# Optimization experiments

Hardware: AMD Instinct MI355X
Metric: run time of the kernel (lower is better)

## Reference

```python
import jax, jax.numpy as jnp
import numpy as np


def _haar_coeffs(x, s):
    # 2x2 depthwise Haar conv at stride s, no padding.
    # Output spatial size = floor((H-2)/s)+1 = len(range(0, H-1, s)).
    H, W = x.shape[-2], x.shape[-1]
    x00 = x[..., 0:H - 1:s, 0:W - 1:s]
    x01 = x[..., 0:H - 1:s, 1:W:s]
    x10 = x[..., 1:H:s, 0:W - 1:s]
    x11 = x[..., 1:H:s, 1:W:s]
    ll = (x00 + x01 + x10 + x11) * 0.25
    lh = (x00 + x01 - x10 - x11) * 0.25
    hl = (x00 - x01 + x10 - x11) * 0.25
    hh = (x00 - x01 - x10 + x11) * 0.25
    return ll, lh, hl, hh


def _resize_hw(x, H, W):
    # bilinear, half-pixel centers == torch align_corners=False (upsampling)
    return jax.image.resize(x, x.shape[:-2] + (H, W), method='linear')


def setup_inputs() -> dict:
    key = jax.random.key(0)
    x = jax.random.normal(key, (8, 64, 256, 256), dtype=jnp.float32)
    return {"x": x, "level": 2}


def reference(x, level):
    B, C, H, W = x.shape
    low_freq = x
    high_freq = jnp.zeros_like(x)
    for l in range(level):
        stride = 2 ** l
        if H // stride < 2 or W // stride < 2:
            break
        ll, lh, hl, hh = _haar_coeffs(low_freq, stride)
        current_high = jnp.abs(lh) + jnp.abs(hl) + jnp.abs(hh)
        high_freq = high_freq + _resize_hw(current_high, H, W)
        low_freq = _resize_hw(ll, H, W)
    if level > 0:
        high_freq = high_freq / level
    return (low_freq, high_freq)
```

## Files before the change

kernel.cpp:

```cpp
#include <hip/hip_runtime.h>


constexpr int IW = 256, IH = 256;

__device__ __forceinline__ float lerpf(float a, float b, float t) {
  return a + t * (b - a);
}

__global__ __launch_bounds__(256)
void haar_fused(const float* __restrict__ x,
                float* __restrict__ out_low,
                float* __restrict__ out_high) {
  const int bc = blockIdx.y;
  const int ti = blockIdx.x >> 2;
  const int tj = blockIdx.x & 3;
  const int i0 = ti * 64, j0 = tj * 64;
  const int tid = threadIdx.x;
  const int lane = tid & 63;
  const int wid = tid >> 6;
  const float c512 = 1.0f / 512.0f;

  __shared__ float sX[70 * 72];
  __shared__ float sLL1[69 * 69];
  __shared__ float sCH1[65 * 65];
  __shared__ float sLL2[34 * 34];
  __shared__ float sCH2[34 * 34];

  const float* xc = x + (size_t)bc * (IH * IW);

  const int colbase = min(max(j0 - 4, 0), IW - 72);
  const int soff = colbase - j0 + 4;
  for (int idx = tid; idx < 70 * 18; idx += 256) {
    int r = idx / 18;
    int c4 = idx - r * 18;
    int gslot = 4 * c4 + soff;
    if (gslot >= 0 && gslot <= 68) {
      int gr = min(max(i0 - 3 + r, 0), IH - 1);
      const float4 v = *reinterpret_cast<const float4*>(&xc[gr * IW + colbase + 4 * c4]);
      *reinterpret_cast<float4*>(&sX[r * 72 + gslot]) = v;
    }
  }
  if (soff != 0) {
    __syncthreads();
    if (tid < 70) {
      if (soff > 0) {
        float v = sX[tid * 72 + 4];
        sX[tid * 72 + 0] = v; sX[tid * 72 + 1] = v;
        sX[tid * 72 + 2] = v; sX[tid * 72 + 3] = v;
      } else {
        float v = sX[tid * 72 + 67];
        sX[tid * 72 + 68] = v; sX[tid * 72 + 69] = v;
        sX[tid * 72 + 70] = v; sX[tid * 72 + 71] = v;
      }
    }
  }
  __syncthreads();

  {
    int r0 = wid * 18;
    int r1 = min(r0 + 18, 69);
    int xc0 = lane + 1;
    float a = sX[r0 * 72 + xc0], b = sX[r0 * 72 + xc0 + 1];
    float s = a + b, d = a - b;
    for (int xr = r0; xr < r1; ++xr) {
      float a2 = sX[(xr + 1) * 72 + xc0], b2 = sX[(xr + 1) * 72 + xc0 + 1];
      float s2 = a2 + b2, d2 = a2 - b2;
      sLL1[xr * 69 + lane] = 0.25f * (s + s2);
      float lh = 0.25f * (s - s2);
      float hl = 0.25f * (d + d2);
      float hh = 0.25f * (d - d2);
      float ch = fabsf(lh) + fabsf(hl) + fabsf(hh);
      if (lane >= 2 && (unsigned)(xr - 2) <= 64u)
        sCH1[(xr - 2) * 65 + (lane - 2)] = ch;
      s = s2; d = d2;
    }
  }
  for (int f = tid; f < 5 * 69; f += 256) {
    int q = f / 69;
    int xr = f - q * 69;
    int xc0 = 65 + q;
    float a = sX[xr * 72 + xc0], b = sX[xr * 72 + xc0 + 1];
    float a2 = sX[(xr + 1) * 72 + xc0], b2 = sX[(xr + 1) * 72 + xc0 + 1];
    float s = a + b, d = a - b, s2 = a2 + b2, d2 = a2 - b2;
    sLL1[xr * 69 + (xc0 - 1)] = 0.25f * (s + s2);
    if (xc0 <= 67 && (unsigned)(xr - 2) <= 64u) {
      float lh = 0.25f * (s - s2);
      float hl = 0.25f * (d + d2);
      float hh = 0.25f * (d - d2);
      sCH1[(xr - 2) * 65 + (xc0 - 3)] = fabsf(lh) + fabsf(hl) + fabsf(hh);
    }
  }
  __syncthreads();

  {
    int fcc = lane;
    int C = j0 - 2 + fcc;
    float ccf = (float)C - (float)(2 * C + 1) * c512;
    float fc = fminf(fmaxf(ccf, 0.0f), 254.0f) - (float)(C - 1);
    int r0 = wid * 17, r1 = r0 + 17;
    float A = sLL1[r0 * 69 + fcc], B = sLL1[r0 * 69 + fcc + 1];
    float hz = A + fc * (B - A);
    for (int fr = r0; fr < r1; ++fr) {
      float A2 = sLL1[(fr + 1) * 69 + fcc], B2 = sLL1[(fr + 1) * 69 + fcc + 1];
      float hz2 = A2 + fc * (B2 - A2);
      int R = i0 - 2 + fr;
      float crf = (float)R - (float)(2 * R + 1) * c512;
      float fw = fminf(fmaxf(crf, 0.0f), 254.0f) - (float)(R - 1);
      sX[fr * 68 + fcc] = hz + fw * (hz2 - hz);
      hz = hz2;
    }
  }
  for (int f = tid; f < 4 * 68; f += 256) {
    int q = f / 68;
    int fr = f - q * 68;
    int fcc = 64 + q;
    int C = j0 - 2 + fcc;
    float ccf = (float)C - (float)(2 * C + 1) * c512;
    float fc = fminf(fmaxf(ccf, 0.0f), 254.0f) - (float)(C - 1);
    float A = sLL1[fr * 69 + fcc], B = sLL1[fr * 69 + fcc + 1];
    float A2 = sLL1[(fr + 1) * 69 + fcc], B2 = sLL1[(fr + 1) * 69 + fcc + 1];
    int R = i0 - 2 + fr;
    float crf = (float)R - (float)(2 * R + 1) * c512;
    float fw = fminf(fmaxf(crf, 0.0f), 254.0f) - (float)(R - 1);
    float hz = A + fc * (B - A);
    float hz2 = A2 + fc * (B2 - A2);
    sX[fr * 68 + fcc] = hz + fw * (hz2 - hz);
  }
  __syncthreads();

  for (int idx = tid; idx < 34 * 32; idx += 256) {
    int pr = idx >> 5, pc = idx & 31;
    int base = (2 * pr) * 68 + 2 * pc;
    float f00 = sX[base], f01 = sX[base + 1];
    float f10 = sX[base + 68], f11 = sX[base + 69];
    float sa = f00 + f01, sb = f10 + f11;
    float da = f00 - f01, db = f10 - f11;
    sLL2[pr * 34 + pc] = 0.25f * (sa + sb);
    sCH2[pr * 34 + pc] =
        fabsf(0.25f * (sa - sb)) + fabsf(0.25f * (da + db)) + fabsf(0.25f * (da - db));
  }
  if (tid < 68) {
    int pr = tid >> 1, pc = 32 + (tid & 1);
    int base = (2 * pr) * 68 + 2 * pc;
    float f00 = sX[base], f01 = sX[base + 1];
    float f10 = sX[base + 68], f11 = sX[base + 69];
    float sa = f00 + f01, sb = f10 + f11;
    float da = f00 - f01, db = f10 - f11;
    sLL2[pr * 34 + pc] = 0.25f * (sa + sb);
    sCH2[pr * 34 + pc] =
        fabsf(0.25f * (sa - sb)) + fabsf(0.25f * (da + db)) + fabsf(0.25f * (da - db));
  }
  __syncthreads();

  {
    const int cg = tid & 15, rb = tid >> 4;
    const int cbase = 4 * cg;
    const int q0 = (j0 >> 1) - 1;
    const int p0 = (i0 >> 1) - 1;
    float fc1[4], fc2[4];
#pragma unroll
    for (int m = 0; m < 4; ++m) {
      int jj = j0 + cbase + m;
      float ccf = (float)jj - (float)(2 * jj + 1) * c512;
      fc1[m] = fminf(fmaxf(ccf, 0.0f), 254.0f) - (float)(jj - 1);
      int qu = (jj - 1) >> 1;
      fc2[m] = fminf(fmaxf(0.5f * (float)jj - 0.25f, 0.0f), 127.0f) - (float)qu;
    }
    const int qs0 = ((j0 + cbase - 1) >> 1) - q0;
    const size_t obase = (size_t)bc * (IH * IW);

#pragma unroll
    for (int k = 0; k < 4; ++k) {
      int r = rb + 16 * k;
      int i = i0 + r;
      float crf = (float)i - (float)(2 * i + 1) * c512;
      float fr1 = fminf(fmaxf(crf, 0.0f), 254.0f) - (float)(i - 1);
      int pu = (i - 1) >> 1;
      float fr2 = fminf(fmaxf(0.5f * (float)i - 0.25f, 0.0f), 127.0f) - (float)pu;
      int ps = pu - p0;

      const float* chA = &sCH1[r * 65 + cbase];
      const float* chB = chA + 65;
      const float* llA = &sLL2[ps * 34 + qs0];
      const float* llB = llA + 34;
      const float* c2A = &sCH2[ps * 34 + qs0];
      const float* c2B = c2A + 34;

      float av[5], bv[5];
#pragma unroll
      for (int m = 0; m < 5; ++m) { av[m] = chA[m]; bv[m] = chB[m]; }
      float lav[4], lbv[4], gav[4], gbv[4];
#pragma unroll
      for (int m = 0; m < 4; ++m) {
        lav[m] = llA[m]; lbv[m] = llB[m];
        gav[m] = c2A[m]; gbv[m] = c2B[m];
      }

      float lo[4], hi[4];
#pragma unroll
      for (int m = 0; m < 4; ++m) {
        const int k2 = (m == 0) ? 0 : (m == 3 ? 2 : 1);
        float h1 = lerpf(lerpf(av[m], av[m + 1], fc1[m]),
                         lerpf(bv[m], bv[m + 1], fc1[m]), fr1);
        float l_ = lerpf(lerpf(lav[k2], lav[k2 + 1], fc2[m]),
                         lerpf(lbv[k2], lbv[k2 + 1], fc2[m]), fr2);
        float h2 = lerpf(lerpf(gav[k2], gav[k2 + 1], fc2[m]),
                         lerpf(gbv[k2], gbv[k2 + 1], fc2[m]), fr2);
        lo[m] = l_;
        hi[m] = 0.5f * (h1 + h2);
      }
      float4 lowv = make_float4(lo[0], lo[1], lo[2], lo[3]);
      float4 highv = make_float4(hi[0], hi[1], hi[2], hi[3]);
      size_t off = obase + (size_t)i * IW + (j0 + cbase);
      *reinterpret_cast<float4*>(&out_low[off]) = lowv;
      *reinterpret_cast<float4*>(&out_high[off]) = highv;
    }
  }
}

extern "C" void kernel_launch(void* const* d_in, const int* in_sizes, int n_in,
                              void* d_out, int out_size, void* d_ws, size_t ws_size,
                              hipStream_t stream) {
  (void)in_sizes; (void)n_in; (void)d_ws; (void)ws_size; (void)out_size;
  const float* x = (const float*)d_in[0];
  float* out_low = (float*)d_out;
  float* out_high = out_low + (size_t)8 * 64 * 256 * 256;

  dim3 grid(16, 512, 1);
  dim3 block(256, 1, 1);
  haar_fused<<<grid, block, 0, stream>>>(x, out_low, out_high);
}
```

Before: 442.2 us.

## Shrink row tile to 32 and fuse level-1 LL with bilinear resize

```diff
diff --git a/kernel.cpp b/kernel.cpp
--- a/kernel.cpp
+++ b/kernel.cpp
@@ -14,27 +14,27 @@
   const int bc = blockIdx.y;
   const int ti = blockIdx.x >> 2;
   const int tj = blockIdx.x & 3;
-  const int i0 = ti * 64, j0 = tj * 64;
+  const int i0 = ti * 32, j0 = tj * 64;
   const int tid = threadIdx.x;
   const int lane = tid & 63;
   const int wid = tid >> 6;
   const float c512 = 1.0f / 512.0f;
 
-  __shared__ float sX[70 * 72];
-  __shared__ float sLL1[69 * 69];
-  __shared__ float sCH1[65 * 65];
-  __shared__ float sLL2[34 * 34];
-  __shared__ float sCH2[34 * 34];
+  __shared__ float sX[38 * 72];
+  __shared__ float sCH1[33 * 68];
+  __shared__ float sLF1[36 * 68];
+  __shared__ float sLL2[18 * 34];
+  __shared__ float sCH2[18 * 34];
 
   const float* xc = x + (size_t)bc * (IH * IW);
 
   const int colbase = min(max(j0 - 4, 0), IW - 72);
   const int soff = colbase - j0 + 4;
-  for (int idx = tid; idx < 70 * 18; idx += 256) {
+  for (int idx = tid; idx < 38 * 18; idx += 256) {
     int r = idx / 18;
     int c4 = idx - r * 18;
     int gslot = 4 * c4 + soff;
-    if (gslot >= 0 && gslot <= 68) {
+    if ((unsigned)gslot <= 68u) {
       int gr = min(max(i0 - 3 + r, 0), IH - 1);
       const float4 v = *reinterpret_cast<const float4*>(&xc[gr * IW + colbase + 4 * c4]);
       *reinterpret_cast<float4*>(&sX[r * 72 + gslot]) = v;
@@ -42,7 +42,7 @@
   }
   if (soff != 0) {
     __syncthreads();
-    if (tid < 70) {
+    if (tid < 38) {
       if (soff > 0) {
         float v = sX[tid * 72 + 4];
         sX[tid * 72 + 0] = v; sX[tid * 72 + 1] = v;
@@ -57,106 +57,94 @@
   __syncthreads();
 
   {
-    int r0 = wid * 18;
-    int r1 = min(r0 + 18, 69);
-    int xc0 = lane + 1;
-    float a = sX[r0 * 72 + xc0], b = sX[r0 * 72 + xc0 + 1];
+    const int r0 = (wid < 3) ? wid * 9 : 27;
+    const int r1 = (wid < 3) ? r0 + 9 : 33;
+    const int xs = lane + 3;
+    float a = sX[(r0 + 2) * 72 + xs], b = sX[(r0 + 2) * 72 + xs + 1];
     float s = a + b, d = a - b;
-    for (int xr = r0; xr < r1; ++xr) {
-      float a2 = sX[(xr + 1) * 72 + xc0], b2 = sX[(xr + 1) * 72 + xc0 + 1];
+    for (int r = r0; r < r1; ++r) {
+      float a2 = sX[(r + 3) * 72 + xs], b2 = sX[(r + 3) * 72 + xs + 1];
       float s2 = a2 + b2, d2 = a2 - b2;
-      sLL1[xr * 69 + lane] = 0.25f * (s + s2);
-      float lh = 0.25f * (s - s2);
-      float hl = 0.25f * (d + d2);
-      float hh = 0.25f * (d - d2);
-      float ch = fabsf(lh) + fabsf(hl) + fabsf(hh);
-      if (lane >= 2 && (unsigned)(xr - 2) <= 64u)
-        sCH1[(xr - 2) * 65 + (lane - 2)] = ch;
+      sCH1[r * 68 + lane] =
+          0.25f * (fabsf(s - s2) + fabsf(d + d2) + fabsf(d - d2));
       s = s2; d = d2;
     }
   }
-  for (int f = tid; f < 5 * 69; f += 256) {
-    int q = f / 69;
-    int xr = f - q * 69;
-    int xc0 = 65 + q;
-    float a = sX[xr * 72 + xc0], b = sX[xr * 72 + xc0 + 1];
-    float a2 = sX[(xr + 1) * 72 + xc0], b2 = sX[(xr + 1) * 72 + xc0 + 1];
+  if (tid < 33) {
+    int r = tid;
+    float a = sX[(r + 2) * 72 + 67], b = sX[(r + 2) * 72 + 68];
+    float a2 = sX[(r + 3) * 72 + 67], b2 = sX[(r + 3) * 72 + 68];
     float s = a + b, d = a - b, s2 = a2 + b2, d2 = a2 - b2;
-    sLL1[xr * 69 + (xc0 - 1)] = 0.25f * (s + s2);
-    if (xc0 <= 67 && (unsigned)(xr - 2) <= 64u) {
-      float lh = 0.25f * (s - s2);
-      float hl = 0.25f * (d + d2);
-      float hh = 0.25f * (d - d2);
-      sCH1[(xr - 2) * 65 + (xc0 - 3)] = fabsf(lh) + fabsf(hl) + fabsf(hh);
-    }
-  }
-  __syncthreads();
+    sCH1[r * 68 + 64] =
+        0.25f * (fabsf(s - s2) + fabsf(d + d2) + fabsf(d - d2));
+  }
 
   {
-    int fcc = lane;
-    int C = j0 - 2 + fcc;
+    const int l = lane;
+    const int C = j0 - 2 + l;
     float ccf = (float)C - (float)(2 * C + 1) * c512;
-    float fc = fminf(fmaxf(ccf, 0.0f), 254.0f) - (float)(C - 1);
-    int r0 = wid * 17, r1 = r0 + 17;
-    float A = sLL1[r0 * 69 + fcc], B = sLL1[r0 * 69 + fcc + 1];
-    float hz = A + fc * (B - A);
-    for (int fr = r0; fr < r1; ++fr) {
-      float A2 = sLL1[(fr + 1) * 69 + fcc], B2 = sLL1[(fr + 1) * 69 + fcc + 1];
-      float hz2 = A2 + fc * (B2 - A2);
+    const float t = fminf(fmaxf(ccf, 0.0f), 254.0f) - (float)(C - 1);
+    const int r0 = wid * 9;
+    const float* rowp = &sX[r0 * 72 + l + 1];
+    float xa = rowp[0], xm = rowp[1], xb = rowp[2];
+    float h0 = 0.5f * ((1.0f - t) * xa + xm + t * xb);
+    xa = rowp[72]; xm = rowp[73]; xb = rowp[74];
+    float h1 = 0.5f * ((1.0f - t) * xa + xm + t * xb);
+    for (int fr = r0; fr < r0 + 9; ++fr) {
+      const float* rp = &sX[(fr + 2) * 72 + l + 1];
+      xa = rp[0]; xm = rp[1]; xb = rp[2];
+      float h2 = 0.5f * ((1.0f - t) * xa + xm + t * xb);
       int R = i0 - 2 + fr;
       float crf = (float)R - (float)(2 * R + 1) * c512;
-      float fw = fminf(fmaxf(crf, 0.0f), 254.0f) - (float)(R - 1);
-      sX[fr * 68 + fcc] = hz + fw * (hz2 - hz);
-      hz = hz2;
-    }
-  }
-  for (int f = tid; f < 4 * 68; f += 256) {
-    int q = f / 68;
-    int fr = f - q * 68;
-    int fcc = 64 + q;
-    int C = j0 - 2 + fcc;
+      float u = fminf(fmaxf(crf, 0.0f), 254.0f) - (float)(R - 1);
+      sLF1[fr * 68 + l] = 0.5f * ((1.0f - u) * h0 + h1 + u * h2);
+      h0 = h1; h1 = h2;
+    }
+  }
+  if (tid < 144) {
+    int fr = tid >> 2, q = tid & 3;
+    int l = 64 + q;
+    int C = j0 - 2 + l;
     float ccf = (float)C - (float)(2 * C + 1) * c512;
-    float fc = fminf(fmaxf(ccf, 0.0f), 254.0f) - (float)(C - 1);
-    float A = sLL1[fr * 69 + fcc], B = sLL1[fr * 69 + fcc + 1];
-    float A2 = sLL1[(fr + 1) * 69 + fcc], B2 = sLL1[(fr + 1) * 69 + fcc + 1];
+    float t = fminf(fmaxf(ccf, 0.0f), 254.0f) - (float)(C - 1);
     int R = i0 - 2 + fr;
     float crf = (float)R - (float)(2 * R + 1) * c512;
-    float fw = fminf(fmaxf(crf, 0.0f), 254.0f) - (float)(R - 1);
-    float hz = A + fc * (B - A);
-    float hz2 = A2 + fc * (B2 - A2);
-    sX[fr * 68 + fcc] = hz + fw * (hz2 - hz);
+    float u = fminf(fmaxf(crf, 0.0f), 254.0f) - (float)(R - 1);
+    float h[3];
+#pragma unroll
+    for (int rr = 0; rr < 3; ++rr) {
+      const float* rp = &sX[(fr + rr) * 72 + l + 1];
+      h[rr] = 0.5f * ((1.0f - t) * rp[0] + rp[1] + t * rp[2]);
+    }
+    sLF1[fr * 68 + l] = 0.5f * ((1.0f - u) * h[0] + h[1] + u * h[2]);
   }
   __syncthreads();
 
-  for (int idx = tid; idx < 34 * 32; idx += 256) {
+  for (int idx = tid; idx < 18 * 32; idx += 256) {
     int pr = idx >> 5, pc = idx & 31;
-    int base = (2 * pr) * 68 + 2 * pc;
-    float f00 = sX[base], f01 = sX[base + 1];
-    float f10 = sX[base + 68], f11 = sX[base + 69];
-    float sa = f00 + f01, sb = f10 + f11;
-    float da = f00 - f01, db = f10 - f11;
+    const float2 f0 = *reinterpret_cast<const float2*>(&sLF1[(2 * pr) * 68 + 2 * pc]);
+    const float2 f1 = *reinterpret_cast<const float2*>(&sLF1[(2 * pr + 1) * 68 + 2 * pc]);
+    float sa = f0.x + f0.y, sb = f1.x + f1.y;
+    float da = f0.x - f0.y, db = f1.x - f1.y;
     sLL2[pr * 34 + pc] = 0.25f * (sa + sb);
     sCH2[pr * 34 + pc] =
-        fabsf(0.25f * (sa - sb)) + fabsf(0.25f * (da + db)) + fabsf(0.25f * (da - db));
-  }
-  if (tid < 68) {
+        0.25f * (fabsf(sa - sb) + fabsf(da + db) + fabsf(da - db));
+  }
+  if (tid < 36) {
     int pr = tid >> 1, pc = 32 + (tid & 1);
-    int base = (2 * pr) * 68 + 2 * pc;
-    float f00 = sX[base], f01 = sX[base + 1];
-    float f10 = sX[base + 68], f11 = sX[base + 69];
-    float sa = f00 + f01, sb = f10 + f11;
-    float da = f00 - f01, db = f10 - f11;
+    const float2 f0 = *reinterpret_cast<const float2*>(&sLF1[(2 * pr) * 68 + 2 * pc]);
+    const float2 f1 = *reinterpret_cast<const float2*>(&sLF1[(2 * pr + 1) * 68 + 2 * pc]);
+    float sa = f0.x + f0.y, sb = f1.x + f1.y;
+    float da = f0.x - f0.y, db = f1.x - f1.y;
     sLL2[pr * 34 + pc] = 0.25f * (sa + sb);
     sCH2[pr * 34 + pc] =
-        fabsf(0.25f * (sa - sb)) + fabsf(0.25f * (da + db)) + fabsf(0.25f * (da - db));
+        0.25f * (fabsf(sa - sb) + fabsf(da + db) + fabsf(da - db));
   }
   __syncthreads();
 
   {
     const int cg = tid & 15, rb = tid >> 4;
     const int cbase = 4 * cg;
-    const int q0 = (j0 >> 1) - 1;
-    const int p0 = (i0 >> 1) - 1;
     float fc1[4], fc2[4];
 #pragma unroll
     for (int m = 0; m < 4; ++m) {
@@ -166,21 +154,21 @@
       int qu = (jj - 1) >> 1;
       fc2[m] = fminf(fmaxf(0.5f * (float)jj - 0.25f, 0.0f), 127.0f) - (float)qu;
     }
-    const int qs0 = ((j0 + cbase - 1) >> 1) - q0;
+    const int qs0 = (cbase + 1) >> 1;
     const size_t obase = (size_t)bc * (IH * IW);
 
 #pragma unroll
-    for (int k = 0; k < 4; ++k) {
+    for (int k = 0; k < 2; ++k) {
       int r = rb + 16 * k;
       int i = i0 + r;
       float crf = (float)i - (float)(2 * i + 1) * c512;
       float fr1 = fminf(fmaxf(crf, 0.0f), 254.0f) - (float)(i - 1);
       int pu = (i - 1) >> 1;
       float fr2 = fminf(fmaxf(0.5f * (float)i - 0.25f, 0.0f), 127.0f) - (float)pu;
-      int ps = pu - p0;
-
-      const float* chA = &sCH1[r * 65 + cbase];
-      const float* chB = chA + 65;
+      int ps = (r + 1) >> 1;
+
+      const float* chA = &sCH1[r * 68 + cbase];
+      const float* chB = chA + 68;
       const float* llA = &sLL2[ps * 34 + qs0];
       const float* llB = llA + 34;
       const float* c2A = &sCH2[ps * 34 + qs0];
@@ -226,7 +214,7 @@
   float* out_low = (float*)d_out;
   float* out_high = out_low + (size_t)8 * 64 * 256 * 256;
 
-  dim3 grid(16, 512, 1);
+  dim3 grid(32, 512, 1);
   dim3 block(256, 1, 1);
   haar_fused<<<grid, block, 0, stream>>>(x, out_low, out_high);
 }
```

Measured after the change: 390.3 us. 1.13x faster.
